# Kernel optimization log

Measured on AMD Instinct MI355X. Metric: run time of the kernel, lower is better.

The kernel has to match this reference:

```python
import jax, jax.numpy as jnp
import numpy as np

N, E = 100000, 1600000
IN, ED, H, HL, OUT = 32, 8, 16, 64, 4
BN_EPS = 1e-5


def setup_inputs() -> dict:
    key = jax.random.key(0)
    keys = iter(jax.random.split(key, 64))

    def rn(*s):
        return jax.random.normal(next(keys), s, jnp.float32) * 0.1

    inp = {}
    inp["x"] = jax.random.normal(next(keys), (N, IN), jnp.float32)
    inp["edge_index"] = jax.random.randint(next(keys), (2, E), 0, N)
    inp["edge_attr"] = jax.random.normal(next(keys), (E, ED), jnp.float32)
    for c, din in ((1, IN), (2, H), (3, H)):
        inp[f"ew{c}"] = rn(ED, din)   # GINEConv edge lin: edge_dim -> in_channels
        inp[f"eb{c}"] = rn(din)
        inp[f"wa{c}"] = rn(din, H)    # nn Linear 1
        inp[f"ba{c}"] = rn(H)
        inp[f"g{c}"] = jnp.ones((H,), jnp.float32)    # BN gamma
        inp[f"be{c}"] = jnp.zeros((H,), jnp.float32)  # BN beta
        inp[f"m{c}"] = rn(H)                           # BN running mean
        inp[f"v{c}"] = jax.random.uniform(next(keys), (H,), jnp.float32, 0.5, 1.5)  # BN running var
        inp[f"wb{c}"] = rn(H, H)      # nn Linear 2
        inp[f"bb{c}"] = rn(H)
    inp["lw1"] = rn(3 * H, HL)
    inp["lb1"] = rn(HL)
    inp["lw2"] = rn(HL, OUT)
    inp["lb2"] = rn(OUT)
    return inp


def gine_conv(x, edge_attr, src, dst, ew, eb, wa, ba, g, be, m, v, wb, bb):
    # message: relu(x_j + lin_edge(edge_attr)); aggregate: sum at dst; eps = 0
    e = edge_attr @ ew + eb                      # [E, din]
    msg = jax.nn.relu(x[src] + e)                # [E, din]
    agg = jax.ops.segment_sum(msg, dst, num_segments=x.shape[0])  # [N, din]
    h = (x + agg) @ wa + ba                      # Linear 1
    h = (h - m) * jax.lax.rsqrt(v + BN_EPS) * g + be  # BatchNorm1d (eval)
    h = jax.nn.relu(h)
    h = jax.nn.relu(h @ wb + bb)                 # Linear 2 + ReLU
    return h


def reference(x, edge_index, edge_attr,
              ew1, eb1, wa1, ba1, g1, be1, m1, v1, wb1, bb1,
              ew2, eb2, wa2, ba2, g2, be2, m2, v2, wb2, bb2,
              ew3, eb3, wa3, ba3, g3, be3, m3, v3, wb3, bb3,
              lw1, lb1, lw2, lb2):
    src, dst = edge_index[0], edge_index[1]
    h1 = gine_conv(x, edge_attr, src, dst, ew1, eb1, wa1, ba1, g1, be1, m1, v1, wb1, bb1)
    h2 = gine_conv(h1, edge_attr, src, dst, ew2, eb2, wa2, ba2, g2, be2, m2, v2, wb2, bb2)
    h3 = gine_conv(h2, edge_attr, src, dst, ew3, eb3, wa3, ba3, g3, be3, m3, v3, wb3, bb3)
    h = jnp.concatenate((h1, h2, h3), axis=1)    # [N, 3H]
    h = jax.nn.relu(h @ lw1 + lb1)               # dropout p=0.5 is identity in eval
    return h @ lw2 + lb2                         # [N, OUT]
```

## Files before the change

kernel.cpp:

```cpp
#include <hip/hip_runtime.h>
#include <hip/hip_bf16.h>

#define BN_EPS 1e-5f
#define BINSHIFT 6
#define BINW 64
#define NBLK 256


__global__ __launch_bounds__(256)
void hist2d_kernel(const int* __restrict__ dst, int* __restrict__ histmat,
                   int E, int nbins, int chunk) {
    __shared__ int h[2048];
    for (int i = threadIdx.x; i < nbins; i += 256) h[i] = 0;
    __syncthreads();
    int b = blockIdx.x;
    int e0 = b * chunk;
    int e1 = min(E, e0 + chunk);
    for (int e = e0 + threadIdx.x; e < e1; e += 256)
        atomicAdd(&h[dst[e] >> BINSHIFT], 1);
    __syncthreads();
    int* row = histmat + (size_t)b * nbins;
    for (int i = threadIdx.x; i < nbins; i += 256) row[i] = h[i];
}

__global__ __launch_bounds__(256)
void colsum_kernel(const int* __restrict__ histmat, int* __restrict__ bincnt,
                   int nbins) {
    int bin = blockIdx.x * 256 + threadIdx.x;
    if (bin >= nbins) return;
    int s = 0;
    for (int r = 0; r < NBLK; ++r) s += histmat[(size_t)r * nbins + bin];
    bincnt[bin] = s;
}

__global__ __launch_bounds__(1024)
void bin_scan_kernel(const int* __restrict__ bincnt, int* __restrict__ binstart,
                     int nbins, int E) {
    __shared__ int a[2048];
    __shared__ int b[1024];
    int t = threadIdx.x;
    a[t]        = (t < nbins) ? bincnt[t] : 0;
    a[t + 1024] = (t + 1024 < nbins) ? bincnt[t + 1024] : 0;
    __syncthreads();
    b[t] = a[2 * t] + a[2 * t + 1];
    __syncthreads();
    for (int off = 1; off < 1024; off <<= 1) {
        int v = (t >= off) ? b[t - off] : 0;
        __syncthreads();
        b[t] += v;
        __syncthreads();
    }
    int base = (t == 0) ? 0 : b[t - 1];
    if (2 * t < nbins)     binstart[2 * t]     = base;
    if (2 * t + 1 < nbins) binstart[2 * t + 1] = base + a[2 * t];
    if (t == 0) binstart[nbins] = E;
}

__global__ __launch_bounds__(256)
void rowscan_kernel(int* __restrict__ histmat, const int* __restrict__ binstart,
                    int nbins) {
    __shared__ int a[NBLK];
    int b = blockIdx.x;
    int t = threadIdx.x;
    int v = histmat[(size_t)t * nbins + b];
    a[t] = v;
    __syncthreads();
    for (int off = 1; off < NBLK; off <<= 1) {
        int add = (t >= off) ? a[t - off] : 0;
        __syncthreads();
        a[t] += add;
        __syncthreads();
    }
    histmat[(size_t)t * nbins + b] = binstart[b] + a[t] - v;
}

__global__ __launch_bounds__(256)
void place_kernel(const int* __restrict__ src, const int* __restrict__ dst,
                  const int* __restrict__ histmat, int2* __restrict__ tmp_meta,
                  int E, int nbins, int chunk) {
    __shared__ int cur[2048];
    int b = blockIdx.x;
    const int* row = histmat + (size_t)b * nbins;
    for (int i = threadIdx.x; i < nbins; i += 256) cur[i] = row[i];
    __syncthreads();
    int e0 = b * chunk;
    int e1 = min(E, e0 + chunk);
    for (int e = e0 + threadIdx.x; e < e1; e += 256) {
        int d = dst[e];
        int bin = d >> BINSHIFT;
        int pos = atomicAdd(&cur[bin], 1);
        int2 m;
        m.x = ((d & (BINW - 1)) << 20) | src[e];
        m.y = e;
        tmp_meta[pos] = m;
    }
}

__global__ __launch_bounds__(256)
void pass2_kernel(const int* __restrict__ binstart, const int2* __restrict__ tmp_meta,
                  const float* __restrict__ edge_attr,
                  int* __restrict__ rowstart, int* __restrict__ src_sorted,
                  float* __restrict__ ea_sorted, int N, int E, int nbins) {
    __shared__ int s_cur[BINW];
    int b = blockIdx.x;
    int node0 = b << BINSHIFT;
    int e0 = binstart[b], e1 = binstart[b + 1];
    int t = threadIdx.x;

    if (t < BINW) s_cur[t] = 0;
    __syncthreads();

    for (int e = e0 + t; e < e1; e += 256)
        atomicAdd(&s_cur[tmp_meta[e].x >> 20], 1);
    __syncthreads();

    if (t < BINW) {
        int val = s_cur[t];
        int inc = val;
#pragma unroll
        for (int off = 1; off < 64; off <<= 1) {
            int n = __shfl_up(inc, off);
            if (t >= off) inc += n;
        }
        int excl = e0 + inc - val;
        s_cur[t] = excl;
        int node = node0 + t;
        if (node <= N) rowstart[node] = excl;
    }
    __syncthreads();

    for (int e = e0 + t; e < e1; e += 256) {
        int2 m = tmp_meta[e];
        int dl   = m.x >> 20;
        int srcv = m.x & 0xFFFFF;
        int eid  = m.y;
        int fpos = atomicAdd(&s_cur[dl], 1);
        src_sorted[fpos] = srcv;
        const float4* sp = (const float4*)(edge_attr + (size_t)eid * 8);
        float4 a0 = sp[0], a1 = sp[1];
        float4* dp = (float4*)(ea_sorted + (size_t)fpos * 8);
        dp[0] = a0;
        dp[1] = a1;
    }
}

template<int DIN, int LPN>
__global__ __launch_bounds__(256)
void gine_layer(const float* __restrict__ xin,
                const int*   __restrict__ rowstart,
                const int*   __restrict__ src_sorted,
                const float* __restrict__ ea_sorted,
                const float* __restrict__ ew, const float* __restrict__ eb,
                const float* __restrict__ wa, const float* __restrict__ ba,
                const float* __restrict__ g, const float* __restrict__ be,
                const float* __restrict__ m, const float* __restrict__ v,
                const float* __restrict__ wb, const float* __restrict__ bb,
                float* __restrict__ hout, int N) {
    static_assert(DIN / LPN == 4, "4 channels per lane");
    constexpr int NPB = 256 / LPN;
    constexpr int OC  = 16 / LPN;

    __shared__ float s_wa[DIN * 16];
    __shared__ float s_wb[16 * 16];
    __shared__ float s_ba[16], s_scale[16], s_shift[16], s_bb[16];
    __shared__ float s_s[NPB][DIN + 1];
    __shared__ float s_h[NPB][17];

    int t = threadIdx.x;
    for (int idx = t; idx < DIN * 16; idx += 256) s_wa[idx] = wa[idx];
    s_wb[t] = wb[t];
    if (t < 16) {
        s_ba[t] = ba[t];
        float sc = g[t] * rsqrtf(v[t] + BN_EPS);
        s_scale[t] = sc;
        s_shift[t] = be[t] - m[t] * sc;
        s_bb[t] = bb[t];
    }

    int nl   = t / LPN;
    int lane = t % LPN;
    int i    = blockIdx.x * NPB + nl;
    int c0   = lane * 4;

    float ew_r[8][4];
#pragma unroll
    for (int k = 0; k < 8; ++k) {
        float4 w = *(const float4*)(ew + k * DIN + c0);
        ew_r[k][0] = w.x; ew_r[k][1] = w.y; ew_r[k][2] = w.z; ew_r[k][3] = w.w;
    }
    float4 ebv = *(const float4*)(eb + c0);
    float eb_r[4] = {ebv.x, ebv.y, ebv.z, ebv.w};

    float acc[4] = {0.f, 0.f, 0.f, 0.f};
    if (i < N) {
        int e0 = rowstart[i];
        int e1 = rowstart[i + 1];
        for (int e = e0; e < e1; ++e) {
            int s = src_sorted[e];
            const float4* eap = (const float4*)(ea_sorted + (size_t)e * 8);
            float4 a0 = eap[0], a1 = eap[1];
            float4 xv = *(const float4*)(xin + (size_t)s * DIN + c0);
            float av[8] = {a0.x, a0.y, a0.z, a0.w, a1.x, a1.y, a1.z, a1.w};
            float xr[4] = {xv.x, xv.y, xv.z, xv.w};
#pragma unroll
            for (int j = 0; j < 4; ++j) {
                float lin = eb_r[j];
#pragma unroll
                for (int k = 0; k < 8; ++k) lin = fmaf(av[k], ew_r[k][j], lin);
                float msg = xr[j] + lin;
                acc[j] += (msg > 0.f ? msg : 0.f);
            }
        }
        float4 xi = *(const float4*)(xin + (size_t)i * DIN + c0);
        s_s[nl][c0 + 0] = xi.x + acc[0];
        s_s[nl][c0 + 1] = xi.y + acc[1];
        s_s[nl][c0 + 2] = xi.z + acc[2];
        s_s[nl][c0 + 3] = xi.w + acc[3];
    }
    __syncthreads();

    if (i < N) {
#pragma unroll
        for (int o = 0; o < OC; ++o) {
            int j = lane * OC + o;
            float a = s_ba[j];
#pragma unroll
            for (int k = 0; k < DIN; ++k) a = fmaf(s_s[nl][k], s_wa[k * 16 + j], a);
            a = a * s_scale[j] + s_shift[j];
            s_h[nl][j] = a > 0.f ? a : 0.f;
        }
    }
    __syncthreads();

    if (i < N) {
        float o_[OC];
#pragma unroll
        for (int o = 0; o < OC; ++o) {
            int j = lane * OC + o;
            float a = s_bb[j];
#pragma unroll
            for (int k = 0; k < 16; ++k) a = fmaf(s_h[nl][k], s_wb[k * 16 + j], a);
            o_[o] = a > 0.f ? a : 0.f;
        }
        if constexpr (OC == 4) {
            float4 ov = {o_[0], o_[1], o_[2], o_[3]};
            *(float4*)(hout + (size_t)i * 16 + lane * 4) = ov;
        } else {
            float2 ov = {o_[0], o_[1]};
            *(float2*)(hout + (size_t)i * 16 + lane * 2) = ov;
        }
    }
}

__global__ __launch_bounds__(256)
void final_kernel(const float* __restrict__ h1, const float* __restrict__ h2,
                  const float* __restrict__ h3,
                  const float* __restrict__ lw1, const float* __restrict__ lb1,
                  const float* __restrict__ lw2, const float* __restrict__ lb2,
                  float* __restrict__ out, int N) {
    constexpr int NPB = 64;
    __shared__ float s_lw1[48 * 64];
    __shared__ float s_lw2[64 * 4];
    __shared__ float s_lb1[64];
    __shared__ float s_lb2[4];
    __shared__ float s_c[NPB][49];

    int t = threadIdx.x;
    for (int idx = t; idx < 48 * 64; idx += 256) s_lw1[idx] = lw1[idx];
    s_lw2[t] = lw2[t];
    if (t < 64) s_lb1[t] = lb1[t];
    if (t < 4) s_lb2[t] = lb2[t];

    int nl = t >> 2;
    int l  = t & 3;
    int i  = blockIdx.x * NPB + nl;

    if (i < N) {
        float4 c1 = ((const float4*)(h1 + (size_t)i * 16))[l];
        float4 c2 = ((const float4*)(h2 + (size_t)i * 16))[l];
        float4 c3 = ((const float4*)(h3 + (size_t)i * 16))[l];
        s_c[nl][l * 4 + 0] = c1.x; s_c[nl][l * 4 + 1] = c1.y;
        s_c[nl][l * 4 + 2] = c1.z; s_c[nl][l * 4 + 3] = c1.w;
        s_c[nl][16 + l * 4 + 0] = c2.x; s_c[nl][16 + l * 4 + 1] = c2.y;
        s_c[nl][16 + l * 4 + 2] = c2.z; s_c[nl][16 + l * 4 + 3] = c2.w;
        s_c[nl][32 + l * 4 + 0] = c3.x; s_c[nl][32 + l * 4 + 1] = c3.y;
        s_c[nl][32 + l * 4 + 2] = c3.z; s_c[nl][32 + l * 4 + 3] = c3.w;
    }
    __syncthreads();

    float o0 = 0.f, o1 = 0.f, o2 = 0.f, o3 = 0.f;
    if (i < N) {
#pragma unroll 4
        for (int jj = 0; jj < 16; ++jj) {
            int j = l * 16 + jj;
            float a = s_lb1[j];
#pragma unroll
            for (int k = 0; k < 48; ++k) a = fmaf(s_c[nl][k], s_lw1[k * 64 + j], a);
            a = a > 0.f ? a : 0.f;
            o0 = fmaf(a, s_lw2[j * 4 + 0], o0);
            o1 = fmaf(a, s_lw2[j * 4 + 1], o1);
            o2 = fmaf(a, s_lw2[j * 4 + 2], o2);
            o3 = fmaf(a, s_lw2[j * 4 + 3], o3);
        }
    }
    o0 += __shfl_xor(o0, 1); o0 += __shfl_xor(o0, 2);
    o1 += __shfl_xor(o1, 1); o1 += __shfl_xor(o1, 2);
    o2 += __shfl_xor(o2, 1); o2 += __shfl_xor(o2, 2);
    o3 += __shfl_xor(o3, 1); o3 += __shfl_xor(o3, 2);
    if (i < N && l == 0) {
        float4 o = {o0 + s_lb2[0], o1 + s_lb2[1], o2 + s_lb2[2], o3 + s_lb2[3]};
        *(float4*)(out + (size_t)i * 4) = o;
    }
}

extern "C" void kernel_launch(void* const* d_in, const int* in_sizes, int n_in,
                              void* d_out, int out_size, void* d_ws, size_t ws_size,
                              hipStream_t stream) {
    const float* x  = (const float*)d_in[0];
    const int*   ei = (const int*)d_in[1];
    const float* ea = (const float*)d_in[2];
    const int N = in_sizes[0] / 32;
    const int E = in_sizes[1] / 2;
    const int* srci = ei;
    const int* dsti = ei + E;

    const float* lw1 = (const float*)d_in[33];
    const float* lb1 = (const float*)d_in[34];
    const float* lw2 = (const float*)d_in[35];
    const float* lb2 = (const float*)d_in[36];

    const int nbins = (N + BINW - 1) >> BINSHIFT;
    const int chunk = (E + NBLK - 1) / NBLK;

    char* p = (char*)d_ws;
    int*   binstart   = (int*)p;   p += (size_t)(nbins + 1 + 3) / 4 * 16;
    int*   bincnt     = (int*)p;   p += (size_t)(nbins + 3) / 4 * 16;
    int*   rowstart   = (int*)p;   p += (size_t)(N + 1 + 3) / 4 * 16;
    int*   histmat    = (int*)p;   p += (size_t)NBLK * nbins * 4;
    int*   src_sorted = (int*)p;   p += (size_t)E * 4;
    float* ea_sorted  = (float*)p; p += (size_t)E * 8 * 4;
    char*  u          = p;
    int2*  tmp_meta   = (int2*)u;
    float* h1         = (float*)u;
    float* h2         = h1 + (size_t)N * 16;
    float* h3         = h2 + (size_t)N * 16;

    hist2d_kernel<<<NBLK, 256, 0, stream>>>(dsti, histmat, E, nbins, chunk);
    colsum_kernel<<<(nbins + 255) / 256, 256, 0, stream>>>(histmat, bincnt, nbins);
    bin_scan_kernel<<<1, 1024, 0, stream>>>(bincnt, binstart, nbins, E);
    rowscan_kernel<<<nbins, NBLK, 0, stream>>>(histmat, binstart, nbins);
    place_kernel<<<NBLK, 256, 0, stream>>>(srci, dsti, histmat, tmp_meta,
                                           E, nbins, chunk);
    pass2_kernel<<<nbins, 256, 0, stream>>>(binstart, tmp_meta, ea,
                                            rowstart, src_sorted, ea_sorted,
                                            N, E, nbins);

    gine_layer<32, 8><<<(N + 31) / 32, 256, 0, stream>>>(
        x, rowstart, src_sorted, ea_sorted,
        (const float*)d_in[3], (const float*)d_in[4],
        (const float*)d_in[5], (const float*)d_in[6],
        (const float*)d_in[7], (const float*)d_in[8],
        (const float*)d_in[9], (const float*)d_in[10],
        (const float*)d_in[11], (const float*)d_in[12], h1, N);

    gine_layer<16, 4><<<(N + 63) / 64, 256, 0, stream>>>(
        h1, rowstart, src_sorted, ea_sorted,
        (const float*)d_in[13], (const float*)d_in[14],
        (const float*)d_in[15], (const float*)d_in[16],
        (const float*)d_in[17], (const float*)d_in[18],
        (const float*)d_in[19], (const float*)d_in[20],
        (const float*)d_in[21], (const float*)d_in[22], h2, N);

    gine_layer<16, 4><<<(N + 63) / 64, 256, 0, stream>>>(
        h2, rowstart, src_sorted, ea_sorted,
        (const float*)d_in[23], (const float*)d_in[24],
        (const float*)d_in[25], (const float*)d_in[26],
        (const float*)d_in[27], (const float*)d_in[28],
        (const float*)d_in[29], (const float*)d_in[30],
        (const float*)d_in[31], (const float*)d_in[32], h3, N);

    final_kernel<<<(N + 63) / 64, 256, 0, stream>>>(
        h1, h2, h3, lw1, lb1, lw2, lb2, (float*)d_out, N);
}
```

Before: 550.6 us.

## Replace per-node CSR with bin-level edge processing and shared-memory atomic aggregation

Drops the second sorting pass that built per-node CSR order. Edge attributes are now permuted in bin order by a simple gather kernel. Each GINE layer processes one 64-node bin per block, with edges spread evenly across threads, two at a time, and messages accumulated into shared memory with atomics. This removes the per-node load imbalance of the serial edge loop and the extra sort pass, at the cost of shared-memory atomic contention and a bigger workspace that no longer aliases tmp_meta with the h buffers.

```diff
diff --git a/kernel.cpp b/kernel.cpp
--- a/kernel.cpp
+++ b/kernel.cpp
@@ -97,76 +97,44 @@
 }
 
 __global__ __launch_bounds__(256)
-void pass2_kernel(const int* __restrict__ binstart, const int2* __restrict__ tmp_meta,
-                  const float* __restrict__ edge_attr,
-                  int* __restrict__ rowstart, int* __restrict__ src_sorted,
-                  float* __restrict__ ea_sorted, int N, int E, int nbins) {
-    __shared__ int s_cur[BINW];
-    int b = blockIdx.x;
-    int node0 = b << BINSHIFT;
-    int e0 = binstart[b], e1 = binstart[b + 1];
-    int t = threadIdx.x;
-
-    if (t < BINW) s_cur[t] = 0;
-    __syncthreads();
-
-    for (int e = e0 + t; e < e1; e += 256)
-        atomicAdd(&s_cur[tmp_meta[e].x >> 20], 1);
-    __syncthreads();
-
-    if (t < BINW) {
-        int val = s_cur[t];
-        int inc = val;
-#pragma unroll
-        for (int off = 1; off < 64; off <<= 1) {
-            int n = __shfl_up(inc, off);
-            if (t >= off) inc += n;
-        }
-        int excl = e0 + inc - val;
-        s_cur[t] = excl;
-        int node = node0 + t;
-        if (node <= N) rowstart[node] = excl;
-    }
-    __syncthreads();
-
-    for (int e = e0 + t; e < e1; e += 256) {
-        int2 m = tmp_meta[e];
-        int dl   = m.x >> 20;
-        int srcv = m.x & 0xFFFFF;
-        int eid  = m.y;
-        int fpos = atomicAdd(&s_cur[dl], 1);
-        src_sorted[fpos] = srcv;
-        const float4* sp = (const float4*)(edge_attr + (size_t)eid * 8);
-        float4 a0 = sp[0], a1 = sp[1];
-        float4* dp = (float4*)(ea_sorted + (size_t)fpos * 8);
-        dp[0] = a0;
-        dp[1] = a1;
-    }
+void permute_ea_kernel(const float* __restrict__ edge_attr,
+                       const int2* __restrict__ tmp_meta,
+                       float* __restrict__ ea_sorted, int E) {
+    int e = blockIdx.x * 256 + threadIdx.x;
+    if (e >= E) return;
+    int eid = tmp_meta[e].y;
+    const float4* sp = (const float4*)(edge_attr + (size_t)eid * 8);
+    float4 a0 = sp[0], a1 = sp[1];
+    float4* dp = (float4*)(ea_sorted + (size_t)e * 8);
+    dp[0] = a0;
+    dp[1] = a1;
 }
 
 template<int DIN, int LPN>
 __global__ __launch_bounds__(256)
-void gine_layer(const float* __restrict__ xin,
-                const int*   __restrict__ rowstart,
-                const int*   __restrict__ src_sorted,
-                const float* __restrict__ ea_sorted,
-                const float* __restrict__ ew, const float* __restrict__ eb,
-                const float* __restrict__ wa, const float* __restrict__ ba,
-                const float* __restrict__ g, const float* __restrict__ be,
-                const float* __restrict__ m, const float* __restrict__ v,
-                const float* __restrict__ wb, const float* __restrict__ bb,
-                float* __restrict__ hout, int N) {
+void gine_layer_bin(const float* __restrict__ xin,
+                    const int*   __restrict__ binstart,
+                    const int2*  __restrict__ tmp_meta,
+                    const float* __restrict__ ea_sorted,
+                    const float* __restrict__ ew, const float* __restrict__ eb,
+                    const float* __restrict__ wa, const float* __restrict__ ba,
+                    const float* __restrict__ g, const float* __restrict__ be,
+                    const float* __restrict__ m, const float* __restrict__ v,
+                    const float* __restrict__ wb, const float* __restrict__ bb,
+                    float* __restrict__ hout,
+                    int N) {
     static_assert(DIN / LPN == 4, "4 channels per lane");
-    constexpr int NPB = 256 / LPN;
-    constexpr int OC  = 16 / LPN;
-
+    constexpr int EPB = 256 / LPN;
+    constexpr int PAD = DIN + 1;
+
+    __shared__ float s_agg[BINW * PAD];
     __shared__ float s_wa[DIN * 16];
     __shared__ float s_wb[16 * 16];
     __shared__ float s_ba[16], s_scale[16], s_shift[16], s_bb[16];
-    __shared__ float s_s[NPB][DIN + 1];
-    __shared__ float s_h[NPB][17];
+    __shared__ float s_h[BINW * 17];
 
     int t = threadIdx.x;
+    for (int idx = t; idx < BINW * PAD; idx += 256) s_agg[idx] = 0.f;
     for (int idx = t; idx < DIN * 16; idx += 256) s_wa[idx] = wa[idx];
     s_wb[t] = wb[t];
     if (t < 16) {
@@ -177,10 +145,9 @@
         s_bb[t] = bb[t];
     }
 
-    int nl   = t / LPN;
-    int lane = t % LPN;
-    int i    = blockIdx.x * NPB + nl;
-    int c0   = lane * 4;
+    int group = t / LPN;
+    int lane  = t % LPN;
+    int c0    = lane * 4;
 
     float ew_r[8][4];
 #pragma unroll
@@ -191,64 +158,105 @@
     float4 ebv = *(const float4*)(eb + c0);
     float eb_r[4] = {ebv.x, ebv.y, ebv.z, ebv.w};
 
-    float acc[4] = {0.f, 0.f, 0.f, 0.f};
-    if (i < N) {
-        int e0 = rowstart[i];
-        int e1 = rowstart[i + 1];
-        for (int e = e0; e < e1; ++e) {
-            int s = src_sorted[e];
-            const float4* eap = (const float4*)(ea_sorted + (size_t)e * 8);
-            float4 a0 = eap[0], a1 = eap[1];
-            float4 xv = *(const float4*)(xin + (size_t)s * DIN + c0);
-            float av[8] = {a0.x, a0.y, a0.z, a0.w, a1.x, a1.y, a1.z, a1.w};
-            float xr[4] = {xv.x, xv.y, xv.z, xv.w};
-#pragma unroll
-            for (int j = 0; j < 4; ++j) {
-                float lin = eb_r[j];
-#pragma unroll
-                for (int k = 0; k < 8; ++k) lin = fmaf(av[k], ew_r[k][j], lin);
-                float msg = xr[j] + lin;
-                acc[j] += (msg > 0.f ? msg : 0.f);
+    int b = blockIdx.x;
+    int node0 = b << BINSHIFT;
+    int e0 = binstart[b], e1 = binstart[b + 1];
+    __syncthreads();
+
+    for (int base = e0; base < e1; base += 2 * EPB) {
+        int eA = base + group;
+        int eB = eA + EPB;
+        int cA = min(eA, e1 - 1);
+        int cB = min(eB, e1 - 1);
+
+        int2 mA = tmp_meta[cA];
+        int2 mB = tmp_meta[cB];
+        const float4* pA = (const float4*)(ea_sorted + (size_t)cA * 8);
+        const float4* pB = (const float4*)(ea_sorted + (size_t)cB * 8);
+        float4 a0A = pA[0], a1A = pA[1];
+        float4 a0B = pB[0], a1B = pB[1];
+
+        int sA = mA.x & 0xFFFFF, dlA = mA.x >> 20;
+        int sB = mB.x & 0xFFFFF, dlB = mB.x >> 20;
+        float4 xA = *(const float4*)(xin + (size_t)sA * DIN + c0);
+        float4 xB = *(const float4*)(xin + (size_t)sB * DIN + c0);
+
+        float avA[8] = {a0A.x, a0A.y, a0A.z, a0A.w, a1A.x, a1A.y, a1A.z, a1A.w};
+        float avB[8] = {a0B.x, a0B.y, a0B.z, a0B.w, a1B.x, a1B.y, a1B.z, a1B.w};
+        float xrA[4] = {xA.x, xA.y, xA.z, xA.w};
+        float xrB[4] = {xB.x, xB.y, xB.z, xB.w};
+
+        float msgA[4], msgB[4];
+#pragma unroll
+        for (int j = 0; j < 4; ++j) {
+            float la = eb_r[j], lb = eb_r[j];
+#pragma unroll
+            for (int k = 0; k < 8; ++k) {
+                la = fmaf(avA[k], ew_r[k][j], la);
+                lb = fmaf(avB[k], ew_r[k][j], lb);
             }
-        }
-        float4 xi = *(const float4*)(xin + (size_t)i * DIN + c0);
-        s_s[nl][c0 + 0] = xi.x + acc[0];
-        s_s[nl][c0 + 1] = xi.y + acc[1];
-        s_s[nl][c0 + 2] = xi.z + acc[2];
-        s_s[nl][c0 + 3] = xi.w + acc[3];
-    }
-    __syncthreads();
-
-    if (i < N) {
-#pragma unroll
-        for (int o = 0; o < OC; ++o) {
-            int j = lane * OC + o;
+            la += xrA[j];
+            lb += xrB[j];
+            msgA[j] = la > 0.f ? la : 0.f;
+            msgB[j] = lb > 0.f ? lb : 0.f;
+        }
+        if (eA < e1) {
+#pragma unroll
+            for (int j = 0; j < 4; ++j)
+                atomicAdd(&s_agg[dlA * PAD + c0 + j], msgA[j]);
+        }
+        if (eB < e1) {
+#pragma unroll
+            for (int j = 0; j < 4; ++j)
+                atomicAdd(&s_agg[dlB * PAD + c0 + j], msgB[j]);
+        }
+    }
+    __syncthreads();
+
+    int nl = t >> 2;
+    int l  = t & 3;
+    int i  = node0 + nl;
+    constexpr int CPT = DIN / 4;
+
+    if (i < N) {
+#pragma unroll
+        for (int q = 0; q < CPT / 4; ++q) {
+            float4 xv = *(const float4*)(xin + (size_t)i * DIN + l * CPT + q * 4);
+            s_agg[nl * PAD + l * CPT + q * 4 + 0] += xv.x;
+            s_agg[nl * PAD + l * CPT + q * 4 + 1] += xv.y;
+            s_agg[nl * PAD + l * CPT + q * 4 + 2] += xv.z;
+            s_agg[nl * PAD + l * CPT + q * 4 + 3] += xv.w;
+        }
+    }
+    __syncthreads();
+
+    if (i < N) {
+#pragma unroll
+        for (int o = 0; o < 4; ++o) {
+            int j = l * 4 + o;
             float a = s_ba[j];
 #pragma unroll
-            for (int k = 0; k < DIN; ++k) a = fmaf(s_s[nl][k], s_wa[k * 16 + j], a);
+            for (int k = 0; k < DIN; ++k)
+                a = fmaf(s_agg[nl * PAD + k], s_wa[k * 16 + j], a);
             a = a * s_scale[j] + s_shift[j];
-            s_h[nl][j] = a > 0.f ? a : 0.f;
-        }
-    }
-    __syncthreads();
-
-    if (i < N) {
-        float o_[OC];
-#pragma unroll
-        for (int o = 0; o < OC; ++o) {
-            int j = lane * OC + o;
+            s_h[nl * 17 + j] = a > 0.f ? a : 0.f;
+        }
+    }
+    __syncthreads();
+
+    if (i < N) {
+        float o_[4];
+#pragma unroll
+        for (int o = 0; o < 4; ++o) {
+            int j = l * 4 + o;
             float a = s_bb[j];
 #pragma unroll
-            for (int k = 0; k < 16; ++k) a = fmaf(s_h[nl][k], s_wb[k * 16 + j], a);
+            for (int k = 0; k < 16; ++k)
+                a = fmaf(s_h[nl * 17 + k], s_wb[k * 16 + j], a);
             o_[o] = a > 0.f ? a : 0.f;
         }
-        if constexpr (OC == 4) {
-            float4 ov = {o_[0], o_[1], o_[2], o_[3]};
-            *(float4*)(hout + (size_t)i * 16 + lane * 4) = ov;
-        } else {
-            float2 ov = {o_[0], o_[1]};
-            *(float2*)(hout + (size_t)i * 16 + lane * 2) = ov;
-        }
+        float4 ov = {o_[0], o_[1], o_[2], o_[3]};
+        *(float4*)(hout + (size_t)i * 16 + l * 4) = ov;
     }
 }
 
@@ -331,19 +339,17 @@
 
     const int nbins = (N + BINW - 1) >> BINSHIFT;
     const int chunk = (E + NBLK - 1) / NBLK;
+    const int eblocks = (E + 255) / 256;
 
     char* p = (char*)d_ws;
     int*   binstart   = (int*)p;   p += (size_t)(nbins + 1 + 3) / 4 * 16;
     int*   bincnt     = (int*)p;   p += (size_t)(nbins + 3) / 4 * 16;
-    int*   rowstart   = (int*)p;   p += (size_t)(N + 1 + 3) / 4 * 16;
     int*   histmat    = (int*)p;   p += (size_t)NBLK * nbins * 4;
-    int*   src_sorted = (int*)p;   p += (size_t)E * 4;
+    int2*  tmp_meta   = (int2*)p;  p += (size_t)E * 8;
     float* ea_sorted  = (float*)p; p += (size_t)E * 8 * 4;
-    char*  u          = p;
-    int2*  tmp_meta   = (int2*)u;
-    float* h1         = (float*)u;
-    float* h2         = h1 + (size_t)N * 16;
-    float* h3         = h2 + (size_t)N * 16;
+    float* h1         = (float*)p; p += (size_t)N * 16 * 4;
+    float* h2         = (float*)p; p += (size_t)N * 16 * 4;
+    float* h3         = (float*)p; p += (size_t)N * 16 * 4;
 
     hist2d_kernel<<<NBLK, 256, 0, stream>>>(dsti, histmat, E, nbins, chunk);
     colsum_kernel<<<(nbins + 255) / 256, 256, 0, stream>>>(histmat, bincnt, nbins);
@@ -351,28 +357,26 @@
     rowscan_kernel<<<nbins, NBLK, 0, stream>>>(histmat, binstart, nbins);
     place_kernel<<<NBLK, 256, 0, stream>>>(srci, dsti, histmat, tmp_meta,
                                            E, nbins, chunk);
-    pass2_kernel<<<nbins, 256, 0, stream>>>(binstart, tmp_meta, ea,
-                                            rowstart, src_sorted, ea_sorted,
-                                            N, E, nbins);
-
-    gine_layer<32, 8><<<(N + 31) / 32, 256, 0, stream>>>(
-        x, rowstart, src_sorted, ea_sorted,
+    permute_ea_kernel<<<eblocks, 256, 0, stream>>>(ea, tmp_meta, ea_sorted, E);
+
+    gine_layer_bin<32, 8><<<nbins, 256, 0, stream>>>(
+        x, binstart, tmp_meta, ea_sorted,
         (const float*)d_in[3], (const float*)d_in[4],
         (const float*)d_in[5], (const float*)d_in[6],
         (const float*)d_in[7], (const float*)d_in[8],
         (const float*)d_in[9], (const float*)d_in[10],
         (const float*)d_in[11], (const float*)d_in[12], h1, N);
 
-    gine_layer<16, 4><<<(N + 63) / 64, 256, 0, stream>>>(
-        h1, rowstart, src_sorted, ea_sorted,
+    gine_layer_bin<16, 4><<<nbins, 256, 0, stream>>>(
+        h1, binstart, tmp_meta, ea_sorted,
         (const float*)d_in[13], (const float*)d_in[14],
         (const float*)d_in[15], (const float*)d_in[16],
         (const float*)d_in[17], (const float*)d_in[18],
         (const float*)d_in[19], (const float*)d_in[20],
         (const float*)d_in[21], (const float*)d_in[22], h2, N);
 
-    gine_layer<16, 4><<<(N + 63) / 64, 256, 0, stream>>>(
-        h2, rowstart, src_sorted, ea_sorted,
+    gine_layer_bin<16, 4><<<nbins, 256, 0, stream>>>(
+        h2, binstart, tmp_meta, ea_sorted,
         (const float*)d_in[23], (const float*)d_in[24],
         (const float*)d_in[25], (const float*)d_in[26],
         (const float*)d_in[27], (const float*)d_in[28],
```

Result: slower. 914.9 us (+66.2%).

## Split node edge lists across lanes with shuffle reduction in GINE layers

Applied to the files above, without the earlier changes.

Each 64-lane wave now handles four nodes in turn, and S lanes share one node's edge list, striding over its edges. Partial sums are combined with xor shuffles before the dense MLP stage, which now maps one thread per (node, output channel). This aims to cut the serial per-node edge loop (about 16 edges per node) and raise memory-level parallelism on the gathers. The cost is more blocks with only 16 nodes each, repeated weight loads into shared memory per block, and shuffle overhead.

```diff
diff --git a/kernel.cpp b/kernel.cpp
--- a/kernel.cpp
+++ b/kernel.cpp
@@ -144,27 +144,27 @@
     }
 }
 
-template<int DIN, int LPN>
-__global__ __launch_bounds__(256)
-void gine_layer(const float* __restrict__ xin,
-                const int*   __restrict__ rowstart,
-                const int*   __restrict__ src_sorted,
-                const float* __restrict__ ea_sorted,
-                const float* __restrict__ ew, const float* __restrict__ eb,
-                const float* __restrict__ wa, const float* __restrict__ ba,
-                const float* __restrict__ g, const float* __restrict__ be,
-                const float* __restrict__ m, const float* __restrict__ v,
-                const float* __restrict__ wb, const float* __restrict__ bb,
-                float* __restrict__ hout, int N) {
-    static_assert(DIN / LPN == 4, "4 channels per lane");
-    constexpr int NPB = 256 / LPN;
-    constexpr int OC  = 16 / LPN;
+template<int DIN, int C, int S>
+__global__ __launch_bounds__(256)
+void gine_layer_wave(const float* __restrict__ xin,
+                     const int*   __restrict__ rowstart,
+                     const int*   __restrict__ src_sorted,
+                     const float* __restrict__ ea_sorted,
+                     const float* __restrict__ ew, const float* __restrict__ eb,
+                     const float* __restrict__ wa, const float* __restrict__ ba,
+                     const float* __restrict__ g, const float* __restrict__ be,
+                     const float* __restrict__ m, const float* __restrict__ v,
+                     const float* __restrict__ wb, const float* __restrict__ bb,
+                     float* __restrict__ hout,
+                     int N) {
+    static_assert(C * S == 64 && C * 4 == DIN, "lane layout");
+    constexpr int PAD = DIN + 1;
 
     __shared__ float s_wa[DIN * 16];
-    __shared__ float s_wb[16 * 16];
+    __shared__ float s_wb[256];
     __shared__ float s_ba[16], s_scale[16], s_shift[16], s_bb[16];
-    __shared__ float s_s[NPB][DIN + 1];
-    __shared__ float s_h[NPB][17];
+    __shared__ float s_s[16 * PAD];
+    __shared__ float s_h[16 * 17];
 
     int t = threadIdx.x;
     for (int idx = t; idx < DIN * 16; idx += 256) s_wa[idx] = wa[idx];
@@ -177,79 +177,80 @@
         s_bb[t] = bb[t];
     }
 
-    int nl   = t / LPN;
-    int lane = t % LPN;
-    int i    = blockIdx.x * NPB + nl;
-    int c0   = lane * 4;
+    int w    = t >> 6;
+    int lane = t & 63;
+    int c    = lane / S;
+    int s    = lane % S;
+    int c0   = c * 4;
 
     float ew_r[8][4];
 #pragma unroll
     for (int k = 0; k < 8; ++k) {
-        float4 w = *(const float4*)(ew + k * DIN + c0);
-        ew_r[k][0] = w.x; ew_r[k][1] = w.y; ew_r[k][2] = w.z; ew_r[k][3] = w.w;
+        float4 wv = *(const float4*)(ew + k * DIN + c0);
+        ew_r[k][0] = wv.x; ew_r[k][1] = wv.y; ew_r[k][2] = wv.z; ew_r[k][3] = wv.w;
     }
     float4 ebv = *(const float4*)(eb + c0);
     float eb_r[4] = {ebv.x, ebv.y, ebv.z, ebv.w};
 
-    float acc[4] = {0.f, 0.f, 0.f, 0.f};
-    if (i < N) {
-        int e0 = rowstart[i];
-        int e1 = rowstart[i + 1];
-        for (int e = e0; e < e1; ++e) {
-            int s = src_sorted[e];
-            const float4* eap = (const float4*)(ea_sorted + (size_t)e * 8);
-            float4 a0 = eap[0], a1 = eap[1];
-            float4 xv = *(const float4*)(xin + (size_t)s * DIN + c0);
-            float av[8] = {a0.x, a0.y, a0.z, a0.w, a1.x, a1.y, a1.z, a1.w};
-            float xr[4] = {xv.x, xv.y, xv.z, xv.w};
-#pragma unroll
-            for (int j = 0; j < 4; ++j) {
-                float lin = eb_r[j];
-#pragma unroll
-                for (int k = 0; k < 8; ++k) lin = fmaf(av[k], ew_r[k][j], lin);
-                float msg = xr[j] + lin;
-                acc[j] += (msg > 0.f ? msg : 0.f);
+    int node0 = blockIdx.x * 16;
+
+#pragma unroll
+    for (int q = 0; q < 4; ++q) {
+        int nl = w * 4 + q;
+        int i  = node0 + nl;
+        float acc[4] = {0.f, 0.f, 0.f, 0.f};
+        if (i < N) {
+            int e0 = rowstart[i];
+            int e1 = rowstart[i + 1];
+            for (int e = e0 + s; e < e1; e += S) {
+                int sv = src_sorted[e];
+                const float4* ep = (const float4*)(ea_sorted + (size_t)e * 8);
+                float4 a0 = ep[0], a1 = ep[1];
+                float4 xv = *(const float4*)(xin + (size_t)sv * DIN + c0);
+                float av[8] = {a0.x, a0.y, a0.z, a0.w, a1.x, a1.y, a1.z, a1.w};
+                float xr[4] = {xv.x, xv.y, xv.z, xv.w};
+#pragma unroll
+                for (int j = 0; j < 4; ++j) {
+                    float lin = eb_r[j];
+#pragma unroll
+                    for (int k = 0; k < 8; ++k) lin = fmaf(av[k], ew_r[k][j], lin);
+                    lin += xr[j];
+                    acc[j] += (lin > 0.f ? lin : 0.f);
+                }
             }
         }
-        float4 xi = *(const float4*)(xin + (size_t)i * DIN + c0);
-        s_s[nl][c0 + 0] = xi.x + acc[0];
-        s_s[nl][c0 + 1] = xi.y + acc[1];
-        s_s[nl][c0 + 2] = xi.z + acc[2];
-        s_s[nl][c0 + 3] = xi.w + acc[3];
-    }
-    __syncthreads();
-
-    if (i < N) {
-#pragma unroll
-        for (int o = 0; o < OC; ++o) {
-            int j = lane * OC + o;
-            float a = s_ba[j];
-#pragma unroll
-            for (int k = 0; k < DIN; ++k) a = fmaf(s_s[nl][k], s_wa[k * 16 + j], a);
-            a = a * s_scale[j] + s_shift[j];
-            s_h[nl][j] = a > 0.f ? a : 0.f;
-        }
-    }
-    __syncthreads();
-
-    if (i < N) {
-        float o_[OC];
-#pragma unroll
-        for (int o = 0; o < OC; ++o) {
-            int j = lane * OC + o;
-            float a = s_bb[j];
-#pragma unroll
-            for (int k = 0; k < 16; ++k) a = fmaf(s_h[nl][k], s_wb[k * 16 + j], a);
-            o_[o] = a > 0.f ? a : 0.f;
-        }
-        if constexpr (OC == 4) {
-            float4 ov = {o_[0], o_[1], o_[2], o_[3]};
-            *(float4*)(hout + (size_t)i * 16 + lane * 4) = ov;
-        } else {
-            float2 ov = {o_[0], o_[1]};
-            *(float2*)(hout + (size_t)i * 16 + lane * 2) = ov;
-        }
-    }
+#pragma unroll
+        for (int mask = S >> 1; mask >= 1; mask >>= 1) {
+#pragma unroll
+            for (int j = 0; j < 4; ++j) acc[j] += __shfl_xor(acc[j], mask);
+        }
+        if (s == 0 && i < N) {
+            float4 xi = *(const float4*)(xin + (size_t)i * DIN + c0);
+            s_s[nl * PAD + c0 + 0] = acc[0] + xi.x;
+            s_s[nl * PAD + c0 + 1] = acc[1] + xi.y;
+            s_s[nl * PAD + c0 + 2] = acc[2] + xi.z;
+            s_s[nl * PAD + c0 + 3] = acc[3] + xi.w;
+        }
+    }
+    __syncthreads();
+
+    int nl2 = t >> 4;
+    int j   = t & 15;
+    float a = s_ba[j];
+#pragma unroll
+    for (int k = 0; k < DIN; ++k)
+        a = fmaf(s_s[nl2 * PAD + k], s_wa[k * 16 + j], a);
+    a = a * s_scale[j] + s_shift[j];
+    s_h[nl2 * 17 + j] = a > 0.f ? a : 0.f;
+    __syncthreads();
+
+    float o = s_bb[j];
+#pragma unroll
+    for (int k = 0; k < 16; ++k)
+        o = fmaf(s_h[nl2 * 17 + k], s_wb[k * 16 + j], o);
+    o = o > 0.f ? o : 0.f;
+    int i2 = node0 + nl2;
+    if (i2 < N) hout[(size_t)i2 * 16 + j] = o;
 }
 
 __global__ __launch_bounds__(256)
@@ -355,7 +356,8 @@
                                             rowstart, src_sorted, ea_sorted,
                                             N, E, nbins);
 
-    gine_layer<32, 8><<<(N + 31) / 32, 256, 0, stream>>>(
+    const int lblocks = (N + 15) / 16;
+    gine_layer_wave<32, 8, 8><<<lblocks, 256, 0, stream>>>(
         x, rowstart, src_sorted, ea_sorted,
         (const float*)d_in[3], (const float*)d_in[4],
         (const float*)d_in[5], (const float*)d_in[6],
@@ -363,7 +365,7 @@
         (const float*)d_in[9], (const float*)d_in[10],
         (const float*)d_in[11], (const float*)d_in[12], h1, N);
 
-    gine_layer<16, 4><<<(N + 63) / 64, 256, 0, stream>>>(
+    gine_layer_wave<16, 4, 16><<<lblocks, 256, 0, stream>>>(
         h1, rowstart, src_sorted, ea_sorted,
         (const float*)d_in[13], (const float*)d_in[14],
         (const float*)d_in[15], (const float*)d_in[16],
@@ -371,7 +373,7 @@
         (const float*)d_in[19], (const float*)d_in[20],
         (const float*)d_in[21], (const float*)d_in[22], h2, N);
 
-    gine_layer<16, 4><<<(N + 63) / 64, 256, 0, stream>>>(
+    gine_layer_wave<16, 4, 16><<<lblocks, 256, 0, stream>>>(
         h2, rowstart, src_sorted, ea_sorted,
         (const float*)d_in[23], (const float*)d_in[24],
         (const float*)d_in[25], (const float*)d_in[26],
```

New measurement: 503.4 us. 1.09x faster.
